# Performance work log

Hardware: AMD Instinct MI355X
Metric: run time of the kernel (lower is better)

Reference implementation:

```python
import jax, jax.numpy as jnp
import numpy as np

N = 8192
FEAT = 3
TRIG = 2
SA = 2
H = 64
ACT = 3
NEG = -1.0e9
EPS = 1e-5


def setup_inputs() -> dict:
    key = jax.random.key(0)
    ks = jax.random.split(key, 24)
    s = 0.05
    node_features = jax.random.uniform(ks[0], (N, FEAT), dtype=jnp.float32)
    adj = jax.random.randint(ks[1], (N, N), 0, 2).astype(jnp.float32)
    # ensure self-loops so every row has at least one neighbor
    adj_matrix = jnp.maximum(adj, jnp.eye(N, dtype=jnp.float32))
    trigger_context = jax.random.uniform(ks[2], (TRIG,), dtype=jnp.float32)
    sa_priors = jax.random.normal(ks[3], (N, SA), dtype=jnp.float32)
    p = lambda k, sh: jax.random.normal(k, sh, dtype=jnp.float32) * s
    return {
        "node_features": node_features,
        "adj_matrix": adj_matrix,
        "trigger_context": trigger_context,
        "sa_priors": sa_priors,
        # node_encoder: Linear(5,64) -> ReLU -> Linear(64,64)
        "w1": p(ks[4], (FEAT + TRIG, H)), "b1": jnp.zeros((H,), jnp.float32),
        "w2": p(ks[5], (H, H)), "b2": jnp.zeros((H,), jnp.float32),
        "wq": p(ks[6], (H, H)), "bq": jnp.zeros((H,), jnp.float32),
        "wk": p(ks[7], (H, H)), "bk": jnp.zeros((H,), jnp.float32),
        "wg": p(ks[8], (TRIG, H)), "bg": jnp.zeros((H,), jnp.float32),
        "stateful_bias": jnp.zeros((1,), jnp.float32),
        "wm": p(ks[9], (H, H)), "bm": jnp.zeros((H,), jnp.float32),
        "ln_g": jnp.ones((H,), jnp.float32), "ln_b": jnp.zeros((H,), jnp.float32),
        "wa1": p(ks[10], (H + SA, H)), "ba1": jnp.zeros((H,), jnp.float32),
        "wa2": p(ks[11], (H, ACT)), "ba2": jnp.zeros((ACT,), jnp.float32),
    }


def reference(node_features, adj_matrix, trigger_context, sa_priors,
              w1, b1, w2, b2, wq, bq, wk, bk, wg, bg, stateful_bias,
              wm, bm, ln_g, ln_b, wa1, ba1, wa2, ba2):
    n = node_features.shape[0]
    trig = jnp.broadcast_to(trigger_context[None, :], (n, TRIG))
    x = jnp.concatenate([node_features, trig], axis=1)          # [N, 5]
    h = jax.nn.relu(x @ w1 + b1) @ w2 + b2                       # [N, H]
    q = h @ wq + bq
    k = h @ wk + bk
    scores = (q @ k.T) * (1.0 / np.sqrt(H))                      # [N, N]
    gate_factor = jnp.mean(jax.nn.sigmoid(trigger_context @ wg + bg))
    topo = jnp.where(adj_matrix == 0, jnp.float32(NEG), adj_matrix)
    is_stateful = node_features[:, 2]
    is_reactive = 1.0 - trigger_context[0]
    sb = jnp.outer(is_stateful, is_stateful) * (stateful_bias[0] * is_reactive)
    scores = scores * gate_factor + topo + sb
    attn = jax.nn.softmax(scores, axis=1)                        # [N, N]
    messages = h @ wm + bm
    aggregated = attn @ messages                                 # [N, H]
    z = h + aggregated
    mu = jnp.mean(z, axis=-1, keepdims=True)
    var = jnp.mean(jnp.square(z - mu), axis=-1, keepdims=True)
    emb = (z - mu) * jax.lax.rsqrt(var + EPS) * ln_g + ln_b      # LayerNorm
    ai = jnp.concatenate([emb, sa_priors], axis=1)               # [N, H+2]
    q_values = jax.nn.relu(ai @ wa1 + ba1) @ wa2 + ba2           # [N, 3]
    return q_values
```

## Files before the change

kernel.cpp:

```cpp
#include <hip/hip_runtime.h>
#include <hip/hip_bf16.h>
#include <math.h>

#define N 8192
#define EPSV 1e-05f
#define NSPLIT 16
#define CPS (N / NSPLIT)
#define NTILE (CPS / 64)

typedef short bf16x8 __attribute__((ext_vector_type(8)));
typedef float f32x4 __attribute__((ext_vector_type(4)));
typedef float f32x16 __attribute__((ext_vector_type(16)));
typedef unsigned short u16;
typedef unsigned int u32;

#define WS_SCAL 0
#define WS_H    64
#define WS_ST   (WS_H + N * 64)
#define WS_SBI  (WS_ST + N)
#define WS_DEN  (WS_SBI + N)
#define WS_AGG  (WS_DEN + N)
#define WS_F_END (WS_AGG + N * 64)
#define WU_BASE (WS_F_END * 2)
#define WU_QB (WU_BASE)
#define WU_KB (WU_BASE + N * 64)
#define WU_MB (WU_BASE + 2 * N * 64)
#define WU_MT (WU_BASE + 3 * N * 64)

static __device__ __forceinline__ u16 f2bf(float f) {
    __hip_bfloat16 h = __float2bfloat16(f);
    return *(u16*)&h;
}

#define TILE_BARRIER() asm volatile("s_waitcnt lgkmcnt(0)\n\ts_barrier" ::: "memory")

__global__ void prep_k(const float* __restrict__ tc, const float* __restrict__ wg,
                       const float* __restrict__ bg, const float* __restrict__ sbias,
                       float* __restrict__ scal) {
    int j = threadIdx.x;
    float v = tc[0] * wg[j] + tc[1] * wg[64 + j] + bg[j];
    float g = 1.0f / (1.0f + __expf(-v));
    for (int off = 32; off; off >>= 1) g += __shfl_xor(g, off, 64);
    if (j == 0) {
        scal[0] = 0.125f * (g * (1.0f / 64.0f));
        scal[1] = sbias[0] * (1.0f - tc[0]);
    }
}

__global__ __launch_bounds__(256) void embed_k(
    const float* __restrict__ nf, const float* __restrict__ tc,
    const float* __restrict__ w1, const float* __restrict__ b1,
    const float* __restrict__ w2, const float* __restrict__ b2,
    const float* __restrict__ wq, const float* __restrict__ bq,
    const float* __restrict__ wk, const float* __restrict__ bk,
    const float* __restrict__ wm, const float* __restrict__ bm,
    float* __restrict__ ws)
{
    const int w = threadIdx.x >> 6, lane = threadIdx.x & 63;
    const int row = blockIdx.x * 4 + w;
    __shared__ float ts[4][64], hs[4][64];
    const float qscale = ws[WS_SCAL + 0];
    const float coef   = ws[WS_SCAL + 1];
    const float f0 = nf[row * 3], f1 = nf[row * 3 + 1], f2 = nf[row * 3 + 2];
    const float t0 = tc[0], t1 = tc[1];
    ws[WS_AGG + (size_t)row * 64 + lane] = 0.0f;
    float v = b1[lane];
    v = fmaf(f0, w1[lane], v);
    v = fmaf(f1, w1[64 + lane], v);
    v = fmaf(f2, w1[128 + lane], v);
    v = fmaf(t0, w1[192 + lane], v);
    v = fmaf(t1, w1[256 + lane], v);
    ts[w][lane] = fmaxf(v, 0.0f);
    __syncthreads();
    float hv = b2[lane];
    #pragma unroll 8
    for (int j = 0; j < 64; j++) hv = fmaf(ts[w][j], w2[j * 64 + lane], hv);
    hs[w][lane] = hv;
    ws[WS_H + row * 64 + lane] = hv;
    __syncthreads();
    float qv = bq[lane], kv = bk[lane], mv = bm[lane];
    #pragma unroll 4
    for (int j = 0; j < 64; j++) {
        const float hj = hs[w][j];
        qv = fmaf(hj, wq[j * 64 + lane], qv);
        kv = fmaf(hj, wk[j * 64 + lane], kv);
        mv = fmaf(hj, wm[j * 64 + lane], mv);
    }
    u16* wu = (u16*)ws;
    wu[WU_QB + row * 64 + lane] = f2bf(qv * qscale);
    wu[WU_KB + row * 64 + lane] = f2bf(kv);
    wu[WU_MB + row * 64 + lane] = f2bf(mv);
    if (lane == 0) {
        ws[WS_ST + row]  = f2;
        ws[WS_SBI + row] = f2 * coef;
        ws[WS_DEN + row] = 0.0f;
    }
}

__global__ __launch_bounds__(256) void transp_k(float* __restrict__ ws) {
    const u16* mb = (const u16*)ws + WU_MB;
    u16* mt = (u16*)ws + WU_MT;
    __shared__ __align__(16) u16 tile[64][72];
    const int i0 = blockIdx.x * 64;
    const int t = threadIdx.x;
    {
        const int r = t >> 2, cb = (t & 3) * 16;
        *(uint4*)&tile[r][cb]     = *(const uint4*)&mb[(size_t)(i0 + r) * 64 + cb];
        *(uint4*)&tile[r][cb + 8] = *(const uint4*)&mb[(size_t)(i0 + r) * 64 + cb + 8];
    }
    __syncthreads();
    const int c = t >> 2, rb = (t & 3) * 16;
    u16 tmp[16];
    #pragma unroll
    for (int i = 0; i < 16; i++) tmp[i] = tile[rb + i][c];
    *(uint4*)&mt[(size_t)c * N + i0 + rb]     = *(uint4*)&tmp[0];
    *(uint4*)&mt[(size_t)c * N + i0 + rb + 8] = *(uint4*)&tmp[8];
}

__global__ __launch_bounds__(256, 3) void attn_k(const float* __restrict__ adj,
                                                 float* __restrict__ ws)
{
    const int rb = blockIdx.x, sp = blockIdx.y;
    const int i0 = rb * 128, j0 = sp * CPS;
    const int tid = threadIdx.x;
    const int w = tid >> 6, lane = tid & 63;
    const int hi = lane >> 5, l31 = lane & 31;

    __shared__ __align__(16) u16 ks[2][64][68];
    __shared__ __align__(16) u16 ms[2][64][68];
    __shared__ __align__(16) u16 ps[4][32][40];
    __shared__ float stl[CPS];

    const u16* qb  = (const u16*)ws + WU_QB;
    const u16* kbp = (const u16*)ws + WU_KB;
    const u16* mtp = (const u16*)ws + WU_MT;

    const int sr = tid >> 2, scb = (tid & 3) * 16;

    *(uint4*)&ks[0][sr][scb]     = *(const uint4*)&kbp[(size_t)(j0 + sr) * 64 + scb];
    *(uint4*)&ks[0][sr][scb + 8] = *(const uint4*)&kbp[(size_t)(j0 + sr) * 64 + scb + 8];
    *(uint4*)&ms[0][sr][scb]     = *(const uint4*)&mtp[(size_t)sr * N + j0 + scb];
    *(uint4*)&ms[0][sr][scb + 8] = *(const uint4*)&mtp[(size_t)sr * N + j0 + scb + 8];
    stl[tid]       = ws[WS_ST + j0 + tid];
    stl[tid + 256] = ws[WS_ST + j0 + tid + 256];
    __syncthreads();

    const int q0 = i0 + w * 32;

    const u16* qr = qb + (size_t)(q0 + l31) * 64;
    bf16x8 qf[4];
    #pragma unroll
    for (int s = 0; s < 4; s++) qf[s] = *(const bf16x8*)&qr[s * 16 + hi * 8];

    float sbir[16];
    #pragma unroll
    for (int r = 0; r < 16; r++) {
        const int qv = (r & 3) + 8 * (r >> 2) + 4 * hi;
        sbir[r] = ws[WS_SBI + q0 + qv];
    }

    f32x16 acc[2];
    #pragma unroll
    for (int hb = 0; hb < 2; hb++)
        #pragma unroll
        for (int i = 0; i < 16; i++) acc[hb][i] = 0.0f;
    float den[16];
    #pragma unroll
    for (int r = 0; r < 16; r++) den[r] = 0.0f;

    const float* adjh = adj + (size_t)(q0 + 4 * hi) * N + j0 + l31;

    float ac[16], an[16];
    #pragma unroll
    for (int r = 0; r < 16; r++) {
        const int cr = (r & 3) + 8 * (r >> 2);
        ac[r] = adjh[(size_t)cr * N];
    }

    uint4 rk0, rk1, rm0, rm1;

    for (int t = 0; t < NTILE; t++) {
        const int cur = t & 1;
        #pragma unroll
        for (int kb = 0; kb < 2; kb++) {
            const int loc = t * 64 + kb * 32;

            if (kb == 0 && t + 1 < NTILE) {
                const int jn = j0 + (t + 1) * 64;
                rk0 = *(const uint4*)&kbp[(size_t)(jn + sr) * 64 + scb];
                rk1 = *(const uint4*)&kbp[(size_t)(jn + sr) * 64 + scb + 8];
                rm0 = *(const uint4*)&mtp[(size_t)sr * N + jn + scb];
                rm1 = *(const uint4*)&mtp[(size_t)sr * N + jn + scb + 8];
            }

            if (loc + 32 < CPS) {
                #pragma unroll
                for (int r = 0; r < 16; r++) {
                    const int cr = (r & 3) + 8 * (r >> 2);
                    an[r] = adjh[(size_t)cr * N + loc + 32];
                }
            } else {
                #pragma unroll
                for (int r = 0; r < 16; r++) an[r] = ac[r];
            }

            f32x16 d;
            #pragma unroll
            for (int i = 0; i < 16; i++) d[i] = 0.0f;
            #pragma unroll
            for (int s = 0; s < 4; s++) {
                const bf16x8 kf = *(const bf16x8*)&ks[cur][kb * 32 + l31][s * 16 + hi * 8];
                d = __builtin_amdgcn_mfma_f32_32x32x16_bf16(qf[s], kf, d, 0, 0, 0);
            }

            const float stc = stl[loc + l31];
            #pragma unroll
            for (int r = 0; r < 16; r++) {
                const int qv = (r & 3) + 8 * (r >> 2) + 4 * hi;
                const float p = ac[r] * __expf(fmaf(sbir[r], stc, d[r]));
                den[r] += p;
                ps[w][qv][l31] = f2bf(p);
            }

            #pragma unroll
            for (int s2 = 0; s2 < 2; s2++) {
                const bf16x8 pa = *(const bf16x8*)&ps[w][l31][s2 * 16 + hi * 8];
                #pragma unroll
                for (int hb = 0; hb < 2; hb++) {
                    const bf16x8 mf = *(const bf16x8*)
                        &ms[cur][hb * 32 + l31][kb * 32 + s2 * 16 + hi * 8];
                    acc[hb] = __builtin_amdgcn_mfma_f32_32x32x16_bf16(pa, mf, acc[hb], 0, 0, 0);
                }
            }

            if (kb == 1 && t + 1 < NTILE) {
                *(uint4*)&ks[cur ^ 1][sr][scb]     = rk0;
                *(uint4*)&ks[cur ^ 1][sr][scb + 8] = rk1;
                *(uint4*)&ms[cur ^ 1][sr][scb]     = rm0;
                *(uint4*)&ms[cur ^ 1][sr][scb + 8] = rm1;
            }

            #pragma unroll
            for (int r = 0; r < 16; r++) ac[r] = an[r];
        }
        if (t + 1 < NTILE) TILE_BARRIER();
    }

    #pragma unroll
    for (int r = 0; r < 16; r++) {
        float dv = den[r];
        dv += __shfl_xor(dv, 1, 64);
        dv += __shfl_xor(dv, 2, 64);
        dv += __shfl_xor(dv, 4, 64);
        dv += __shfl_xor(dv, 8, 64);
        dv += __shfl_xor(dv, 16, 64);
        den[r] = dv;
    }
    if (l31 == 0) {
        #pragma unroll
        for (int r = 0; r < 16; r++) {
            const int qv = (r & 3) + 8 * (r >> 2) + 4 * hi;
            unsafeAtomicAdd(&ws[WS_DEN + q0 + qv], den[r]);
        }
    }

    float* aggp = ws + WS_AGG;
    #pragma unroll
    for (int hb = 0; hb < 2; hb++) {
        #pragma unroll
        for (int r = 0; r < 16; r++) {
            const int qv = (r & 3) + 8 * (r >> 2) + 4 * hi;
            unsafeAtomicAdd(&aggp[(size_t)(q0 + qv) * 64 + hb * 32 + l31],
                            acc[hb][r]);
        }
    }
}

__global__ __launch_bounds__(256) void final_k(
    const float* __restrict__ sa, const float* __restrict__ ln_g,
    const float* __restrict__ ln_b,
    const float* __restrict__ wa1, const float* __restrict__ ba1,
    const float* __restrict__ wa2, const float* __restrict__ ba2,
    const float* __restrict__ ws, float* __restrict__ out)
{
    const int w = threadIdx.x >> 6, lane = threadIdx.x & 63;
    const int row = blockIdx.x * 4 + w;
    __shared__ float es[4][64], hs2[4][64];
    const float a = ws[WS_AGG + (size_t)row * 64 + lane];
    const float d = ws[WS_DEN + row];
    const float z = ws[WS_H + row * 64 + lane] + a / d;
    float mu = z;
    for (int off = 32; off; off >>= 1) mu += __shfl_xor(mu, off, 64);
    mu *= (1.0f / 64.0f);
    const float zc = z - mu;
    float var = zc * zc;
    for (int off = 32; off; off >>= 1) var += __shfl_xor(var, off, 64);
    var *= (1.0f / 64.0f);
    const float emb = zc * rsqrtf(var + EPSV) * ln_g[lane] + ln_b[lane];
    es[w][lane] = emb;
    __syncthreads();
    const float sa0 = sa[row * 2], sa1 = sa[row * 2 + 1];
    float hv = ba1[lane];
    #pragma unroll 8
    for (int c = 0; c < 64; c++) hv = fmaf(es[w][c], wa1[c * 64 + lane], hv);
    hv = fmaf(sa0, wa1[64 * 64 + lane], hv);
    hv = fmaf(sa1, wa1[65 * 64 + lane], hv);
    hs2[w][lane] = fmaxf(hv, 0.0f);
    __syncthreads();
    if (lane < 3) {
        float o = ba2[lane];
        for (int u = 0; u < 64; u++) o = fmaf(hs2[w][u], wa2[u * 3 + lane], o);
        out[row * 3 + lane] = o;
    }
}

extern "C" void kernel_launch(void* const* d_in, const int* in_sizes, int n_in,
                              void* d_out, int out_size, void* d_ws, size_t ws_size,
                              hipStream_t stream)
{
    const float* nf  = (const float*)d_in[0];
    const float* adj = (const float*)d_in[1];
    const float* tc  = (const float*)d_in[2];
    const float* sa  = (const float*)d_in[3];
    const float* w1  = (const float*)d_in[4];
    const float* b1  = (const float*)d_in[5];
    const float* w2  = (const float*)d_in[6];
    const float* b2  = (const float*)d_in[7];
    const float* wq  = (const float*)d_in[8];
    const float* bq  = (const float*)d_in[9];
    const float* wk  = (const float*)d_in[10];
    const float* bk  = (const float*)d_in[11];
    const float* wg  = (const float*)d_in[12];
    const float* bg  = (const float*)d_in[13];
    const float* sb  = (const float*)d_in[14];
    const float* wm  = (const float*)d_in[15];
    const float* bm  = (const float*)d_in[16];
    const float* lng = (const float*)d_in[17];
    const float* lnb = (const float*)d_in[18];
    const float* wa1 = (const float*)d_in[19];
    const float* ba1 = (const float*)d_in[20];
    const float* wa2 = (const float*)d_in[21];
    const float* ba2 = (const float*)d_in[22];
    float* ws  = (float*)d_ws;
    float* out = (float*)d_out;

    prep_k<<<1, 64, 0, stream>>>(tc, wg, bg, sb, ws + WS_SCAL);
    embed_k<<<N / 4, 256, 0, stream>>>(nf, tc, w1, b1, w2, b2, wq, bq, wk, bk,
                                       wm, bm, ws);
    transp_k<<<N / 64, 256, 0, stream>>>(ws);
    attn_k<<<dim3(N / 128, NSPLIT), 256, 0, stream>>>(adj, ws);
    final_k<<<N / 4, 256, 0, stream>>>(sa, lng, lnb, wa1, ba1, wa2, ba2, ws, out);
}
```

Baseline: 474.5 us.

## Preload whole K/M column split into swizzled LDS and drop per-tile barriers

The column split count doubles so each block handles 256 columns. The block's entire K and transposed-M slices are now loaded into XOR-swizzled shared memory up front, which removes the double-buffered tile pipeline and its per-tile barriers. Adjacency loads are prefetched two steps ahead, and MFMA sections are wrapped in s_setprio. Occupancy hint drops from 3 to 2 blocks per SM because of the larger LDS footprint, and twice as many partial atomic reductions occur.

New measurement: 465.9 us. About the same (-1.8%).

```diff
diff --git a/kernel.cpp b/kernel.cpp
--- a/kernel.cpp
+++ b/kernel.cpp
@@ -4,9 +4,9 @@
 
 #define N 8192
 #define EPSV 1e-05f
-#define NSPLIT 16
+#define NSPLIT 32
 #define CPS (N / NSPLIT)
-#define NTILE (CPS / 64)
+#define NSTEP (CPS / 32)
 
 typedef short bf16x8 __attribute__((ext_vector_type(8)));
 typedef float f32x4 __attribute__((ext_vector_type(4)));
@@ -31,8 +31,6 @@
     __hip_bfloat16 h = __float2bfloat16(f);
     return *(u16*)&h;
 }
-
-#define TILE_BARRIER() asm volatile("s_waitcnt lgkmcnt(0)\n\ts_barrier" ::: "memory")
 
 __global__ void prep_k(const float* __restrict__ tc, const float* __restrict__ wg,
                        const float* __restrict__ bg, const float* __restrict__ sbias,
@@ -117,7 +115,7 @@
     *(uint4*)&mt[(size_t)c * N + i0 + rb + 8] = *(uint4*)&tmp[8];
 }
 
-__global__ __launch_bounds__(256, 3) void attn_k(const float* __restrict__ adj,
+__global__ __launch_bounds__(256, 2) void attn_k(const float* __restrict__ adj,
                                                  float* __restrict__ ws)
 {
     const int rb = blockIdx.x, sp = blockIdx.y;
@@ -126,8 +124,8 @@
     const int w = tid >> 6, lane = tid & 63;
     const int hi = lane >> 5, l31 = lane & 31;
 
-    __shared__ __align__(16) u16 ks[2][64][68];
-    __shared__ __align__(16) u16 ms[2][64][68];
+    __shared__ __align__(16) u16 ks[256 * 64];
+    __shared__ __align__(16) u16 ms[64 * 256];
     __shared__ __align__(16) u16 ps[4][32][40];
     __shared__ float stl[CPS];
 
@@ -135,14 +133,21 @@
     const u16* kbp = (const u16*)ws + WU_KB;
     const u16* mtp = (const u16*)ws + WU_MT;
 
-    const int sr = tid >> 2, scb = (tid & 3) * 16;
-
-    *(uint4*)&ks[0][sr][scb]     = *(const uint4*)&kbp[(size_t)(j0 + sr) * 64 + scb];
-    *(uint4*)&ks[0][sr][scb + 8] = *(const uint4*)&kbp[(size_t)(j0 + sr) * 64 + scb + 8];
-    *(uint4*)&ms[0][sr][scb]     = *(const uint4*)&mtp[(size_t)sr * N + j0 + scb];
-    *(uint4*)&ms[0][sr][scb + 8] = *(const uint4*)&mtp[(size_t)sr * N + j0 + scb + 8];
-    stl[tid]       = ws[WS_ST + j0 + tid];
-    stl[tid + 256] = ws[WS_ST + j0 + tid + 256];
+    #pragma unroll
+    for (int i = 0; i < 8; i++) {
+        const int id = tid + 256 * i;
+        const int r = id >> 3, c = id & 7;
+        const int off = r * 64 + (((c * 16) ^ ((r & 7) << 4)) >> 1);
+        *(uint4*)&ks[off] = *(const uint4*)&kbp[(size_t)(j0 + r) * 64 + c * 8];
+    }
+    #pragma unroll
+    for (int i = 0; i < 8; i++) {
+        const int id = tid + 256 * i;
+        const int r = id >> 5, c = id & 31;
+        const int off = r * 256 + (((c * 16) ^ ((r & 7) << 4)) >> 1);
+        *(uint4*)&ms[off] = *(const uint4*)&mtp[(size_t)r * N + j0 + c * 8];
+    }
+    stl[tid] = ws[WS_ST + j0 + tid];
     __syncthreads();
 
     const int q0 = i0 + w * 32;
@@ -175,75 +180,60 @@
     for (int r = 0; r < 16; r++) {
         const int cr = (r & 3) + 8 * (r >> 2);
         ac[r] = adjh[(size_t)cr * N];
-    }
-
-    uint4 rk0, rk1, rm0, rm1;
-
-    for (int t = 0; t < NTILE; t++) {
-        const int cur = t & 1;
-        #pragma unroll
-        for (int kb = 0; kb < 2; kb++) {
-            const int loc = t * 64 + kb * 32;
-
-            if (kb == 0 && t + 1 < NTILE) {
-                const int jn = j0 + (t + 1) * 64;
-                rk0 = *(const uint4*)&kbp[(size_t)(jn + sr) * 64 + scb];
-                rk1 = *(const uint4*)&kbp[(size_t)(jn + sr) * 64 + scb + 8];
-                rm0 = *(const uint4*)&mtp[(size_t)sr * N + jn + scb];
-                rm1 = *(const uint4*)&mtp[(size_t)sr * N + jn + scb + 8];
+        an[r] = adjh[(size_t)cr * N + 32];
+    }
+
+    #pragma unroll 2
+    for (int s = 0; s < NSTEP; s++) {
+        const int loc = s * 32;
+
+        const int pl = (s + 2 < NSTEP) ? loc + 64 : loc;
+        float a2[16];
+        #pragma unroll
+        for (int r = 0; r < 16; r++) {
+            const int cr = (r & 3) + 8 * (r >> 2);
+            a2[r] = adjh[(size_t)cr * N + pl];
+        }
+
+        f32x16 d;
+        #pragma unroll
+        for (int i = 0; i < 16; i++) d[i] = 0.0f;
+        __builtin_amdgcn_s_setprio(1);
+        #pragma unroll
+        for (int s4 = 0; s4 < 4; s4++) {
+            const int R = loc + l31;
+            const bf16x8 kf = *(const bf16x8*)
+                &ks[R * 64 + (((s4 * 32 + hi * 16) ^ ((R & 7) << 4)) >> 1)];
+            d = __builtin_amdgcn_mfma_f32_32x32x16_bf16(qf[s4], kf, d, 0, 0, 0);
+        }
+        __builtin_amdgcn_s_setprio(0);
+
+        const float stc = stl[loc + l31];
+        #pragma unroll
+        for (int r = 0; r < 16; r++) {
+            const int qv = (r & 3) + 8 * (r >> 2) + 4 * hi;
+            const float p = ac[r] * __expf(fmaf(sbir[r], stc, d[r]));
+            den[r] += p;
+            ps[w][qv][l31] = f2bf(p);
+        }
+
+        __builtin_amdgcn_s_setprio(1);
+        #pragma unroll
+        for (int s2 = 0; s2 < 2; s2++) {
+            const bf16x8 pa = *(const bf16x8*)&ps[w][l31][s2 * 16 + hi * 8];
+            #pragma unroll
+            for (int hb = 0; hb < 2; hb++) {
+                const int R2 = hb * 32 + l31;
+                const bf16x8 mf = *(const bf16x8*)
+                    &ms[R2 * 256 +
+                        (((loc * 2 + s2 * 32 + hi * 16) ^ ((R2 & 7) << 4)) >> 1)];
+                acc[hb] = __builtin_amdgcn_mfma_f32_32x32x16_bf16(pa, mf, acc[hb], 0, 0, 0);
             }
-
-            if (loc + 32 < CPS) {
-                #pragma unroll
-                for (int r = 0; r < 16; r++) {
-                    const int cr = (r & 3) + 8 * (r >> 2);
-                    an[r] = adjh[(size_t)cr * N + loc + 32];
-                }
-            } else {
-                #pragma unroll
-                for (int r = 0; r < 16; r++) an[r] = ac[r];
-            }
-
-            f32x16 d;
-            #pragma unroll
-            for (int i = 0; i < 16; i++) d[i] = 0.0f;
-            #pragma unroll
-            for (int s = 0; s < 4; s++) {
-                const bf16x8 kf = *(const bf16x8*)&ks[cur][kb * 32 + l31][s * 16 + hi * 8];
-                d = __builtin_amdgcn_mfma_f32_32x32x16_bf16(qf[s], kf, d, 0, 0, 0);
-            }
-
-            const float stc = stl[loc + l31];
-            #pragma unroll
-            for (int r = 0; r < 16; r++) {
-                const int qv = (r & 3) + 8 * (r >> 2) + 4 * hi;
-                const float p = ac[r] * __expf(fmaf(sbir[r], stc, d[r]));
-                den[r] += p;
-                ps[w][qv][l31] = f2bf(p);
-            }
-
-            #pragma unroll
-            for (int s2 = 0; s2 < 2; s2++) {
-                const bf16x8 pa = *(const bf16x8*)&ps[w][l31][s2 * 16 + hi * 8];
-                #pragma unroll
-                for (int hb = 0; hb < 2; hb++) {
-                    const bf16x8 mf = *(const bf16x8*)
-                        &ms[cur][hb * 32 + l31][kb * 32 + s2 * 16 + hi * 8];
-                    acc[hb] = __builtin_amdgcn_mfma_f32_32x32x16_bf16(pa, mf, acc[hb], 0, 0, 0);
-                }
-            }
-
-            if (kb == 1 && t + 1 < NTILE) {
-                *(uint4*)&ks[cur ^ 1][sr][scb]     = rk0;
-                *(uint4*)&ks[cur ^ 1][sr][scb + 8] = rk1;
-                *(uint4*)&ms[cur ^ 1][sr][scb]     = rm0;
-                *(uint4*)&ms[cur ^ 1][sr][scb + 8] = rm1;
-            }
-
-            #pragma unroll
-            for (int r = 0; r < 16; r++) ac[r] = an[r];
-        }
-        if (t + 1 < NTILE) TILE_BARRIER();
+        }
+        __builtin_amdgcn_s_setprio(0);
+
+        #pragma unroll
+        for (int r = 0; r < 16; r++) { ac[r] = an[r]; an[r] = a2[r]; }
     }
 
     #pragma unroll
```
